# Performance work log

Hardware: AMD Instinct MI355X
Metric: run time of the kernel (lower is better)

## Reference

```python
import jax, jax.numpy as jnp
import numpy as np

N_EMBD = 512
N_HEAD = 8
HEAD_DIM = N_EMBD // N_HEAD  # 64
SCALE = HEAD_DIM ** -0.5


def setup_inputs() -> dict:
    key = jax.random.key(0)
    k1, k2, k3 = jax.random.split(key, 3)
    x = jax.random.normal(k1, (2, 2048, N_EMBD), dtype=jnp.float32)
    # torch Linear(n_embd, 3*n_embd, bias=False) -> store as (in, out): y = x @ W
    w_attn = jax.random.normal(k2, (N_EMBD, 3 * N_EMBD), dtype=jnp.float32) * 0.02
    w_proj = jax.random.normal(k3, (N_EMBD, N_EMBD), dtype=jnp.float32) * 0.02
    return {"x": x, "w_attn": w_attn, "w_proj": w_proj}


def reference(x, w_attn, w_proj):
    B, T, C = x.shape
    qkv = x @ w_attn                                   # (B, T, 3C)
    q, k, v = jnp.split(qkv, 3, axis=-1)
    q = q.reshape(B, T, N_HEAD, HEAD_DIM).transpose(0, 2, 1, 3)  # (B,H,T,D)
    k = k.reshape(B, T, N_HEAD, HEAD_DIM).transpose(0, 2, 1, 3)
    v = v.reshape(B, T, N_HEAD, HEAD_DIM).transpose(0, 2, 1, 3)
    # FAITHFUL to source: `weights.fill_(float('-inf'))` overwrites q@k^T*scale
    # in-place, then triu(diagonal=1) keeps -inf strictly above the diagonal and
    # zeros elsewhere. q/k scores are DISCARDED by the original code.
    # Resulting softmax weights are identical across batch/head, so compute a
    # single (T, T) matrix instead of materializing (B, H, T, T).
    mask = jnp.triu(jnp.full((T, T), -jnp.inf, dtype=x.dtype), 1)  # -inf above diag, 0 else
    w = jax.nn.softmax(mask, axis=-1)                  # uniform over positions <= i
    attn = jnp.einsum('ts,bhsd->bhtd', w, v)           # causal running mean of v
    attn = attn.transpose(0, 2, 1, 3).reshape(B, T, C)
    y = attn @ w_proj
    return y
```

## Files before the change

kernel.cpp:

```cpp
#include <hip/hip_runtime.h>

typedef __bf16 bf16x8 __attribute__((ext_vector_type(8)));
typedef float  f32x4  __attribute__((ext_vector_type(4)));

__device__ __forceinline__ unsigned short f2bf(float f) {
    unsigned int u = __float_as_uint(f);
    u += 0x7FFF + ((u >> 16) & 1);
    return (unsigned short)(u >> 16);
}

#define GLD_LDS16(gptr, lptr) \
    __builtin_amdgcn_global_load_lds((const __attribute__((address_space(1))) void*)(gptr), \
                                     (__attribute__((address_space(3))) void*)(lptr), 16, 0, 0)

template<int EPI>
__device__ __forceinline__ void gemm_tile(const unsigned short* __restrict__ A,
                                          const unsigned short* __restrict__ Bt,
                                          void* __restrict__ Cout,
                                          unsigned short* lds,
                                          int bm, int bn)
{
    const int tid  = threadIdx.x;
    const int lane = tid & 63;
    const int w    = tid >> 6;
    const int wm   = w >> 1, wn = w & 1;
    const int arow = lane & 15;
    const int kg   = lane >> 4;

    const int srow   = tid >> 4;
    const int schunk = (tid & 15) ^ srow;
    const unsigned short* gA = A  + (size_t)(bm + srow) * 512 + schunk * 8;
    const unsigned short* gB = Bt + (size_t)(bn + srow) * 512 + schunk * 8;

    auto stage = [&](int buf, int kt) {
        unsigned short* la = lds + buf * 16384;
        unsigned short* lb = la + 8192;
        const int k0 = kt * 128;
        #pragma unroll
        for (int i = 0; i < 4; ++i) {
            GLD_LDS16(gA + (size_t)(i * 16) * 512 + k0, la + i * 2048 + w * 512);
            GLD_LDS16(gB + (size_t)(i * 16) * 512 + k0, lb + i * 2048 + w * 512);
        }
    };

    int offA[2][4], offB[2][4];
    #pragma unroll
    for (int f = 0; f < 2; ++f)
        #pragma unroll
        for (int kk = 0; kk < 4; ++kk) {
            offA[f][kk] = (wm * 32 + f * 16 + arow) * 256 + (((kk * 4 + kg) ^ arow) << 4);
            offB[f][kk] = (wn * 32 + f * 16 + arow) * 256 + (((kk * 4 + kg) ^ arow) << 4);
        }

    stage(0, 0);
    stage(1, 1);

    f32x4 acc[2][2] = {};
    #pragma unroll
    for (int kt = 0; kt < 4; ++kt) {
        const int buf = kt & 1;
        if (kt < 3) asm volatile("s_waitcnt vmcnt(8)" ::: "memory");
        else        asm volatile("s_waitcnt vmcnt(0)" ::: "memory");
        __builtin_amdgcn_s_barrier();
        const char* la = (const char*)(lds + buf * 16384);
        const char* lb = la + 16384;
        #pragma unroll
        for (int kk = 0; kk < 4; ++kk) {
            bf16x8 a0 = *(const bf16x8*)(la + offA[0][kk]);
            bf16x8 a1 = *(const bf16x8*)(la + offA[1][kk]);
            bf16x8 b0 = *(const bf16x8*)(lb + offB[0][kk]);
            bf16x8 b1 = *(const bf16x8*)(lb + offB[1][kk]);
            acc[0][0] = __builtin_amdgcn_mfma_f32_16x16x32_bf16(a0, b0, acc[0][0], 0, 0, 0);
            acc[0][1] = __builtin_amdgcn_mfma_f32_16x16x32_bf16(a0, b1, acc[0][1], 0, 0, 0);
            acc[1][0] = __builtin_amdgcn_mfma_f32_16x16x32_bf16(a1, b0, acc[1][0], 0, 0, 0);
            acc[1][1] = __builtin_amdgcn_mfma_f32_16x16x32_bf16(a1, b1, acc[1][1], 0, 0, 0);
        }
        __builtin_amdgcn_s_barrier();
        if (kt < 2) stage(buf, kt + 2);
    }

    #pragma unroll
    for (int fm = 0; fm < 2; ++fm)
        #pragma unroll
        for (int fn = 0; fn < 2; ++fn) {
            const int row0 = bm + wm * 32 + fm * 16 + kg * 4;
            const int col  = bn + wn * 32 + fn * 16 + arow;
            if (EPI == 0) {
                float* C = (float*)Cout;
                #pragma unroll
                for (int r = 0; r < 4; ++r)
                    C[(size_t)(row0 + r) * 512 + col] = acc[fm][fn][r];
            } else {
                unsigned short* C = (unsigned short*)Cout;
                ushort4 pk;
                pk.x = f2bf(acc[fm][fn][0]);
                pk.y = f2bf(acc[fm][fn][1]);
                pk.z = f2bf(acc[fm][fn][2]);
                pk.w = f2bf(acc[fm][fn][3]);
                *(ushort4*)(&C[(size_t)col * 512 + row0]) = pk;
            }
        }
}

__global__ __launch_bounds__(256) void k1_prep_partial(
    const float* __restrict__ x, const float* __restrict__ w_attn,
    const float* __restrict__ w_proj,
    unsigned short* __restrict__ wv, unsigned short* __restrict__ wpT,
    float* __restrict__ part)
{
    __shared__ float ls[64][65];
    const int bid = blockIdx.x, tid = threadIdx.x;

    if (bid < 64) {
        const int m0 = (bid >> 3) * 64;
        const int j0 = (bid & 7) * 64;
        const int rr = tid >> 4;
        const int c4 = (tid & 15) * 4;
        #pragma unroll
        for (int i = 0; i < 4; ++i) {
            float4 v = *(const float4*)(w_proj + (size_t)(m0 + rr + 16 * i) * 512 + j0 + c4);
            ls[rr + 16 * i][c4 + 0] = v.x;
            ls[rr + 16 * i][c4 + 1] = v.y;
            ls[rr + 16 * i][c4 + 2] = v.z;
            ls[rr + 16 * i][c4 + 3] = v.w;
        }
        __syncthreads();
        const int c    = tid >> 2;
        const int mgrp = (tid & 3) * 16;
        #pragma unroll
        for (int u = 0; u < 4; ++u) {
            const int m = mgrp + u * 4;
            ushort4 o;
            o.x = f2bf(ls[m + 0][c]);
            o.y = f2bf(ls[m + 1][c]);
            o.z = f2bf(ls[m + 2][c]);
            o.w = f2bf(ls[m + 3][c]);
            *(ushort4*)(wpT + (size_t)(j0 + c) * 512 + m0 + m) = o;
        }
    } else if (bid < 128) {
        const int bb = bid - 64;
        #pragma unroll
        for (int i = 0; i < 4; ++i) {
            const int flat = bb * 1024 + i * 256 + tid;
            const int ir = flat >> 7;
            const int m4 = (flat & 127) * 4;
            float4 v = *(const float4*)(w_attn + (size_t)ir * 1536 + 1024 + m4);
            ushort4 o;
            o.x = f2bf(v.x); o.y = f2bf(v.y); o.z = f2bf(v.z); o.w = f2bf(v.w);
            *(ushort4*)(wv + (size_t)ir * 512 + m4) = o;
        }
    } else {
        const int bx = bid - 128;
        const int b  = bx >> 7;
        const int ch = (bx >> 1) & 63;
        const int j  = (bx & 1) * 256 + tid;
        const float* p = x + ((size_t)b * 2048 + ch * 32) * 512 + j;
        float s = 0.f;
        #pragma unroll 8
        for (int t = 0; t < 32; ++t) s += p[(size_t)t * 512];
        part[((size_t)b * 64 + ch) * 512 + j] = s;
    }
}

__global__ __launch_bounds__(256) void k2_smallgemm_finalize(
    const float* __restrict__ x,
    const unsigned short* __restrict__ wv, const unsigned short* __restrict__ wpT,
    const float* __restrict__ part,
    unsigned short* __restrict__ wcT, unsigned short* __restrict__ s16)
{
    __shared__ __align__(16) unsigned short lds[2 * 16384];
    const int bid = blockIdx.x, tid = threadIdx.x;

    if (bid < 64) {
        gemm_tile<1>(wv, wpT, wcT, lds, (bid >> 3) * 64, (bid & 7) * 64);
    } else {
        const int bx = bid - 64;
        const int b  = bx >> 7;
        const int ch = (bx >> 1) & 63;
        const int j  = (bx & 1) * 256 + tid;
        float run = 0.f;
        #pragma unroll 8
        for (int cc = 0; cc < 63; ++cc) {
            float v = part[((size_t)b * 64 + cc) * 512 + j];
            run += (cc < ch) ? v : 0.f;
        }
        const float*    p = x   + ((size_t)b * 2048 + ch * 32) * 512 + j;
        unsigned short* q = s16 + ((size_t)b * 2048 + ch * 32) * 512 + j;
        #pragma unroll 8
        for (int t = 0; t < 32; ++t) {
            run += p[(size_t)t * 512];
            q[(size_t)t * 512] = f2bf(run * (1.0f / (float)(ch * 32 + t + 1)));
        }
    }
}

__global__ __launch_bounds__(256) void k3_biggemm(
    const unsigned short* __restrict__ s16,
    const unsigned short* __restrict__ wcT,
    float* __restrict__ y)
{
    __shared__ __align__(16) unsigned short lds[2 * 16384];
    const int bid  = blockIdx.x;
    const int xcd  = bid & 7;
    const int idx  = bid >> 3;
    const int vy   = xcd * 8 + (idx >> 3);
    const int vx   = idx & 7;
    gemm_tile<0>(s16, wcT, y, lds, vy * 64, vx * 64);
}

extern "C" void kernel_launch(void* const* d_in, const int* in_sizes, int n_in,
                              void* d_out, int out_size, void* d_ws, size_t ws_size,
                              hipStream_t stream)
{
    const float* x      = (const float*)d_in[0];
    const float* w_attn = (const float*)d_in[1];
    const float* w_proj = (const float*)d_in[2];
    float* y = (float*)d_out;

    unsigned short* wv  = (unsigned short*)d_ws;
    unsigned short* wpT = wv  + 512 * 512;
    unsigned short* wcT = wpT + 512 * 512;
    unsigned short* s16 = wcT + 512 * 512;
    float* part = (float*)(s16 + (size_t)4096 * 512);

    k1_prep_partial<<<384, 256, 0, stream>>>(x, w_attn, w_proj, wv, wpT, part);
    k2_smallgemm_finalize<<<320, 256, 0, stream>>>(x, wv, wpT, part, wcT, s16);
    k3_biggemm<<<512, 256, 0, stream>>>(s16, wcT, y);
}
```

Measured before the change: 24.73 us.

## Enlarge big GEMM tile to 128x64 with K-step 64 and 8-stage loop

The final GEMM kernel now computes 128x64 output tiles per block instead of 64x64, halving the grid to 256 blocks. Each wave handles 4x2 MFMA fragments, and the K dimension is processed in eight steps of 64 with double-buffered LDS and a new XOR swizzle. The larger tile raises A/B reuse and cuts redundant loads of the weight matrix. In exchange it uses only 256 blocks on a 256-CU part, which may lower occupancy and latency hiding, and it adds more pipeline iterations and barriers.

Result: slower. 27.02 us (+9.3%).

```diff
diff --git a/kernel.cpp b/kernel.cpp
--- a/kernel.cpp
+++ b/kernel.cpp
@@ -199,13 +199,85 @@
     const unsigned short* __restrict__ wcT,
     float* __restrict__ y)
 {
-    __shared__ __align__(16) unsigned short lds[2 * 16384];
-    const int bid  = blockIdx.x;
-    const int xcd  = bid & 7;
-    const int idx  = bid >> 3;
-    const int vy   = xcd * 8 + (idx >> 3);
-    const int vx   = idx & 7;
-    gemm_tile<0>(s16, wcT, y, lds, vy * 64, vx * 64);
+    __shared__ __align__(16) unsigned short As[2][128 * 64];
+    __shared__ __align__(16) unsigned short Bs[2][64 * 64];
+
+    const int bid = blockIdx.x;
+    const int xcd = bid & 7, idx = bid >> 3;
+    const int mt  = xcd * 4 + (idx >> 3);
+    const int nt  = idx & 7;
+
+    const int tid  = threadIdx.x;
+    const int lane = tid & 63, w = tid >> 6;
+    const int wm   = w >> 1, wn = w & 1;
+    const int arow = lane & 15, kg = lane >> 4;
+
+    const int srow   = tid >> 3;
+    const int schunk = (lane & 7) ^ (lane >> 3);
+    const unsigned short* gA = s16 + (size_t)(mt * 128 + srow) * 512 + schunk * 8;
+    const unsigned short* gB = wcT + (size_t)(nt * 64  + srow) * 512 + schunk * 8;
+
+    auto stage = [&](int buf, int kt) {
+        const int k0 = kt * 64;
+        unsigned short* la = As[buf];
+        unsigned short* lb = Bs[buf];
+        #pragma unroll
+        for (int i = 0; i < 4; ++i)
+            GLD_LDS16(gA + (size_t)(i * 32) * 512 + k0, la + i * 2048 + w * 512);
+        #pragma unroll
+        for (int i = 0; i < 2; ++i)
+            GLD_LDS16(gB + (size_t)(i * 32) * 512 + k0, lb + i * 2048 + w * 512);
+    };
+
+    int offA[4][2], offB[2][2];
+    #pragma unroll
+    for (int f = 0; f < 4; ++f)
+        #pragma unroll
+        for (int kk = 0; kk < 2; ++kk)
+            offA[f][kk] = (wm * 64 + f * 16 + arow) * 128 + (((kk * 4 + kg) ^ (arow & 7)) << 4);
+    #pragma unroll
+    for (int g = 0; g < 2; ++g)
+        #pragma unroll
+        for (int kk = 0; kk < 2; ++kk)
+            offB[g][kk] = (wn * 32 + g * 16 + arow) * 128 + (((kk * 4 + kg) ^ (arow & 7)) << 4);
+
+    stage(0, 0);
+    stage(1, 1);
+
+    f32x4 acc[4][2] = {};
+    #pragma unroll
+    for (int kt = 0; kt < 8; ++kt) {
+        const int buf = kt & 1;
+        if (kt < 7) asm volatile("s_waitcnt vmcnt(6)" ::: "memory");
+        else        asm volatile("s_waitcnt vmcnt(0)" ::: "memory");
+        __builtin_amdgcn_s_barrier();
+        const char* la = (const char*)As[buf];
+        const char* lb = (const char*)Bs[buf];
+        #pragma unroll
+        for (int kk = 0; kk < 2; ++kk) {
+            bf16x8 b0 = *(const bf16x8*)(lb + offB[0][kk]);
+            bf16x8 b1 = *(const bf16x8*)(lb + offB[1][kk]);
+            #pragma unroll
+            for (int f = 0; f < 4; ++f) {
+                bf16x8 af = *(const bf16x8*)(la + offA[f][kk]);
+                acc[f][0] = __builtin_amdgcn_mfma_f32_16x16x32_bf16(af, b0, acc[f][0], 0, 0, 0);
+                acc[f][1] = __builtin_amdgcn_mfma_f32_16x16x32_bf16(af, b1, acc[f][1], 0, 0, 0);
+            }
+        }
+        __builtin_amdgcn_s_barrier();
+        if (kt < 6) stage(buf, kt + 2);
+    }
+
+    #pragma unroll
+    for (int f = 0; f < 4; ++f)
+        #pragma unroll
+        for (int g = 0; g < 2; ++g) {
+            const int row0 = mt * 128 + wm * 64 + f * 16 + kg * 4;
+            const int col  = nt * 64  + wn * 32 + g * 16 + arow;
+            #pragma unroll
+            for (int r = 0; r < 4; ++r)
+                y[(size_t)(row0 + r) * 512 + col] = acc[f][g][r];
+        }
 }
 
 extern "C" void kernel_launch(void* const* d_in, const int* in_sizes, int n_in,
@@ -225,5 +297,5 @@
 
     k1_prep_partial<<<384, 256, 0, stream>>>(x, w_attn, w_proj, wv, wpT, part);
     k2_smallgemm_finalize<<<320, 256, 0, stream>>>(x, wv, wpT, part, wcT, s16);
-    k3_biggemm<<<512, 256, 0, stream>>>(s16, wcT, y);
-}
+    k3_biggemm<<<256, 256, 0, stream>>>(s16, wcT, y);
+}
```
